# Kernel optimization log

Measured on AMD Instinct MI355X. Metric: run time of the kernel, lower is better.

The kernel has to match this reference:

```python
import jax, jax.numpy as jnp
import numpy as np

B, T, C = 4, 2048, 1024
H, D = 16, 64

def setup_inputs() -> dict:
    key = jax.random.key(0)
    k1, k2, k3 = jax.random.split(key, 3)
    x = jax.random.normal(k1, (B, T, C), dtype=jnp.float32)
    Wqkv = jax.random.normal(k2, (C, 3 * C), dtype=jnp.float32) * (1.0 / np.sqrt(C))
    Wproj = jax.random.normal(k3, (C, C), dtype=jnp.float32) * (1.0 / np.sqrt(C))
    return {"x": x, "Wqkv": Wqkv, "Wproj": Wproj}

def reference(x, Wqkv, Wproj):
    Bx, Tx, Cx = x.shape
    qkv = x @ Wqkv                       # (B, T, 3C)
    q, k, v = jnp.split(qkv, 3, axis=-1)
    # (B, T, C) -> (B, H, T, D)
    q = q.reshape(Bx, Tx, H, D).transpose(0, 2, 1, 3)
    k = k.reshape(Bx, Tx, H, D).transpose(0, 2, 1, 3)
    v = v.reshape(Bx, Tx, H, D).transpose(0, 2, 1, 3)
    att = jnp.einsum('bhqd,bhkd->bhqk', q, k) / jnp.sqrt(jnp.float32(D))
    causal = jnp.tril(jnp.ones((Tx, Tx), dtype=bool))  # (T, T)
    att = jnp.where(causal[None, None, :, :], att, jnp.float32(-jnp.inf))
    att = jax.nn.softmax(att, axis=-1)
    y = jnp.einsum('bhqk,bhkd->bhqd', att, v)          # (B, H, T, D)
    y = y.transpose(0, 2, 1, 3).reshape(Bx, Tx, Cx)
    return y @ Wproj
```

## Files before the change

kernel.cpp:

```cpp
#include <hip/hip_runtime.h>
#include <cstdint>
#include <cstddef>


typedef short bf16x8 __attribute__((ext_vector_type(8)));
typedef float f32x4 __attribute__((ext_vector_type(4)));
typedef float f32x16 __attribute__((ext_vector_type(16)));

#define MFMA32(a, b, c) __builtin_amdgcn_mfma_f32_16x16x32_bf16((a), (b), (c), 0, 0, 0)
#define MFMA3216(a, b, c) __builtin_amdgcn_mfma_f32_32x32x16_bf16((a), (b), (c), 0, 0, 0)

__device__ __forceinline__ unsigned short f2b(float f) {
  unsigned int x = __builtin_bit_cast(unsigned int, f);
  x += 0x7fffu + ((x >> 16) & 1u);
  return (unsigned short)(x >> 16);
}

__device__ __forceinline__ unsigned int pack2(float a, float b) {
  return (unsigned int)f2b(a) | ((unsigned int)f2b(b) << 16);
}

__device__ __forceinline__ unsigned int cvtpk(float a, float b) {
  unsigned int r;
  asm("v_cvt_pk_bf16_f32 %0, %1, %2" : "=v"(r) : "v"(a), "v"(b));
  return r;
}

__device__ __forceinline__ float exp2v(float x) {
  float r;
  asm("v_exp_f32 %0, %1" : "=v"(r) : "v"(x));
  return r;
}

__device__ __forceinline__ void gload16(const void* g, void* l) {
  __builtin_amdgcn_global_load_lds(
      (const __attribute__((address_space(1))) void*)g,
      (__attribute__((address_space(3))) void*)l, 16, 0, 0);
}

__global__ __launch_bounds__(256) void k_conv_x(const float* __restrict__ in,
                                                unsigned short* __restrict__ out, int n4) {
  int i = blockIdx.x * 256 + threadIdx.x;
  if (i >= n4) return;
  float4 v = reinterpret_cast<const float4*>(in)[i];
  ushort4 o;
  o.x = f2b(v.x); o.y = f2b(v.y); o.z = f2b(v.z); o.w = f2b(v.w);
  reinterpret_cast<ushort4*>(out)[i] = o;
}

__global__ __launch_bounds__(256) void k_transpose(const float* __restrict__ in,
                                                   unsigned short* __restrict__ out,
                                                   int R, int C) {
  __shared__ float tile[32][33];
  int c0 = blockIdx.x * 32, r0 = blockIdx.y * 32;
  int tx = threadIdx.x & 31, ty = threadIdx.x >> 5;
#pragma unroll
  for (int j = 0; j < 4; ++j)
    tile[ty + 8 * j][tx] = in[(size_t)(r0 + ty + 8 * j) * C + c0 + tx];
  __syncthreads();
#pragma unroll
  for (int j = 0; j < 4; ++j)
    out[(size_t)(c0 + ty + 8 * j) * R + r0 + tx] = f2b(tile[tx][ty + 8 * j]);
}

template <int EPI>
__global__ __launch_bounds__(256, 5) void k_gemm(const unsigned short* __restrict__ A,
                                                 const unsigned short* __restrict__ Bt,
                                                 float* __restrict__ outF,
                                                 unsigned short* __restrict__ q_ws,
                                                 unsigned short* __restrict__ k_ws,
                                                 unsigned short* __restrict__ v_ws,
                                                 int M, int N) {
  constexpr int K = 1024;
  __shared__ unsigned short smem[16384];
  unsigned short* As = smem;
  unsigned short* Bs = smem + 8192;
  const int bn = blockIdx.x, bm = blockIdx.y;
  const int tid = threadIdx.x;
  const int w = tid >> 6, lane = tid & 63;
  const int wm = w >> 1, wn = w & 1;
  const int c = lane & 15, g = lane >> 4;
  const int cl8 = c & 7;

  f32x4 acc[4][4];
#pragma unroll
  for (int i = 0; i < 4; ++i)
#pragma unroll
    for (int j = 0; j < 4; ++j) acc[i][j] = (f32x4){0.f, 0.f, 0.f, 0.f};

  const int srow = 32 * w + (lane >> 3);
  const int scol = 8 * ((lane & 7) ^ (lane >> 3));
  const unsigned short* Ag = A + (size_t)(bm * 128 + srow) * K + scol;
  const unsigned short* Bg = Bt + (size_t)(bn * 128 + srow) * K + scol;
  char* AsB = (char*)As + w * 4096;
  char* BsB = (char*)Bs + w * 4096;

  for (int kt = 0; kt < K / 64; ++kt) {
    const int kb = kt * 64;
    __syncthreads();
#pragma unroll
    for (int i = 0; i < 4; ++i) {
      gload16(Ag + (size_t)(8 * i) * K + kb, AsB + i * 1024);
      gload16(Bg + (size_t)(8 * i) * K + kb, BsB + i * 1024);
    }
    asm volatile("s_waitcnt vmcnt(0)" ::: "memory");
    __syncthreads();
#pragma unroll
    for (int u = 0; u < 2; ++u) {
      bf16x8 af[4], bfr[4];
#pragma unroll
      for (int mf = 0; mf < 4; ++mf)
        af[mf] = *(const bf16x8*)((const char*)As + (wm * 64 + mf * 16 + c) * 128 +
                                  (((u * 4 + g) ^ cl8) * 16));
#pragma unroll
      for (int nf = 0; nf < 4; ++nf)
        bfr[nf] = *(const bf16x8*)((const char*)Bs + (wn * 64 + nf * 16 + c) * 128 +
                                   (((u * 4 + g) ^ cl8) * 16));
#pragma unroll
      for (int mf = 0; mf < 4; ++mf)
#pragma unroll
        for (int nf = 0; nf < 4; ++nf)
          acc[mf][nf] = MFMA32(af[mf], bfr[nf], acc[mf][nf]);
    }
  }

  const int rowb = bm * 128 + wm * 64;
  const int colb = bn * 128 + wn * 64;
  if (EPI == 1) {
#pragma unroll
    for (int mf = 0; mf < 4; ++mf)
#pragma unroll
      for (int nf = 0; nf < 4; ++nf)
#pragma unroll
        for (int r = 0; r < 4; ++r) {
          int row = rowb + mf * 16 + 4 * g + r;
          int col = colb + nf * 16 + c;
          outF[(size_t)row * N + col] = acc[mf][nf][r];
        }
  } else {
    const int sec = colb >> 10;
    const int hh = (colb & 1023) >> 6;
    const int b = rowb >> 11, t0 = rowb & 2047;
    unsigned short* Lw = smem + w * 4096;

    __syncthreads();
    if (sec < 2) {
      const float sc = (sec == 0) ? 0.125f * 1.4426950408889634f : 1.f;
#pragma unroll
      for (int mf = 0; mf < 4; ++mf)
#pragma unroll
        for (int nf = 0; nf < 4; ++nf)
#pragma unroll
          for (int r = 0; r < 4; ++r)
            Lw[(16 * mf + 4 * g + r) * 64 + 16 * nf + c] = f2b(acc[mf][nf][r] * sc);
    } else {
#pragma unroll
      for (int mf = 0; mf < 4; ++mf)
#pragma unroll
        for (int nf = 0; nf < 4; ++nf)
#pragma unroll
          for (int rr = 0; rr < 2; ++rr)
            *(unsigned int*)&Lw[(16 * nf + c) * 64 + 16 * mf + 4 * g + 2 * rr] =
                pack2(acc[mf][nf][2 * rr], acc[mf][nf][2 * rr + 1]);
    }
    asm volatile("s_waitcnt lgkmcnt(0)" ::: "memory");
    const int rw = lane >> 3, ch = lane & 7;
    const int chx = ch ^ rw;
    if (sec == 0) {
      unsigned short* dst = q_ws + ((size_t)(b * 16 + hh) * 2048 + t0) * 64;
#pragma unroll
      for (int i = 0; i < 8; ++i) {
        int tl = i * 8 + rw;
        *(bf16x8*)(dst + (size_t)tl * 64 + ch * 8) = *(const bf16x8*)&Lw[tl * 64 + ch * 8];
      }
    } else if (sec == 1) {
      unsigned short* dst = k_ws + ((size_t)(b * 16 + hh) * 2048 + t0) * 64;
#pragma unroll
      for (int i = 0; i < 8; ++i) {
        int tl = i * 8 + rw;
        *(bf16x8*)(dst + (size_t)tl * 64 + chx * 8) = *(const bf16x8*)&Lw[tl * 64 + ch * 8];
      }
    } else {
      unsigned short* dst = v_ws + (size_t)(b * 16 + hh) * 64 * 2048 + t0;
#pragma unroll
      for (int i = 0; i < 8; ++i) {
        int dl = i * 8 + rw;
        *(bf16x8*)(dst + (size_t)dl * 2048 + chx * 8) = *(const bf16x8*)&Lw[dl * 64 + ch * 8];
      }
    }
  }
}

__global__ __launch_bounds__(256, 4) void k_attn(const unsigned short* __restrict__ q_ws,
                                                 const unsigned short* __restrict__ k_ws,
                                                 const unsigned short* __restrict__ v_ws,
                                                 unsigned short* __restrict__ y_ws) {
  constexpr int T = 2048;
  __shared__ unsigned short Ks[2][64 * 64];
  __shared__ unsigned short Vs[2][64 * 64];
  const int f = blockIdx.x;
  const int r = f >> 3;
  const int bh = (f & 7) * 8 + (r & 7);
  const int xi = 15 - (r >> 3);
  const int tid = threadIdx.x, w = tid >> 6, lane = tid & 63;
  const int q32 = lane & 31;
  const int hi = lane >> 5;
  const int l7 = lane & 7;
  const size_t base = (size_t)bh * T * 64;
  const unsigned short* Kb = k_ws + base;
  const unsigned short* Vb = v_ws + base;
  const unsigned short* Qb = q_ws + base;

  const int srow = w * 16 + (lane >> 3);
  const int sch = lane & 7;

  const int q0 = xi * 128;
  const int qb = q0 + 32 * w;
  const int qcol = qb + q32;
  const int n_kt = (q0 >> 6) + 2;
  bf16x8 qf[4];
#pragma unroll
  for (int ks = 0; ks < 4; ++ks)
    qf[ks] = *(const bf16x8*)(Qb + (size_t)qcol * 64 + 16 * ks + 8 * hi);

  f32x16 yacc[2];
#pragma unroll
  for (int db = 0; db < 2; ++db)
#pragma unroll
    for (int i = 0; i < 16; ++i) yacc[db][i] = 0.f;
  float m_run = -1e30f, l_part = 0.f;

  gload16(Kb + (size_t)srow * 64 + sch * 8, (char*)&Ks[0][0] + w * 2048);
  gload16(Kb + (size_t)(srow + 8) * 64 + sch * 8, (char*)&Ks[0][0] + w * 2048 + 1024);
  gload16(Vb + (size_t)srow * T + sch * 8, (char*)&Vs[0][0] + w * 2048);
  gload16(Vb + (size_t)(srow + 8) * T + sch * 8, (char*)&Vs[0][0] + w * 2048 + 1024);

#pragma unroll 1
  for (int kt = 0; kt < n_kt; ++kt) {
    const int k0 = kt * 64;
    const int cur = kt & 1;
    if (kt + 1 < n_kt) {
      const int k0n = k0 + 64;
      char* KsW = (char*)&Ks[cur ^ 1][0] + w * 2048;
      char* VsW = (char*)&Vs[cur ^ 1][0] + w * 2048;
      gload16(Kb + (size_t)(k0n + srow) * 64 + sch * 8, KsW);
      gload16(Kb + (size_t)(k0n + srow + 8) * 64 + sch * 8, KsW + 1024);
      gload16(Vb + (size_t)srow * T + k0n + sch * 8, VsW);
      gload16(Vb + (size_t)(srow + 8) * T + k0n + sch * 8, VsW + 1024);
      asm volatile("s_waitcnt vmcnt(4)" ::: "memory");
    } else {
      asm volatile("s_waitcnt vmcnt(0)" ::: "memory");
    }
    __builtin_amdgcn_s_barrier();

    if (k0 <= qb + 31) {
      const char* KsC = (const char*)&Ks[cur][0];
      const char* VsC = (const char*)&Vs[cur][0];
      f32x16 s[2];
#pragma unroll
      for (int tb = 0; tb < 2; ++tb)
#pragma unroll
        for (int i = 0; i < 16; ++i) s[tb][i] = 0.f;
      __builtin_amdgcn_s_setprio(1);
#pragma unroll
      for (int ks = 0; ks < 4; ++ks) {
        const int chk = ((2 * ks + hi) ^ l7) * 16;
#pragma unroll
        for (int tb = 0; tb < 2; ++tb) {
          const int row = 32 * tb + q32;
          bf16x8 kf = *(const bf16x8*)(KsC + row * 128 + chk);
          s[tb] = MFMA3216(kf, qf[ks], s[tb]);
        }
      }
      __builtin_amdgcn_s_setprio(0);
      if (k0 + 63 > qb) {
#pragma unroll
        for (int tb = 0; tb < 2; ++tb)
#pragma unroll
          for (int rr = 0; rr < 16; ++rr) {
            int tk = k0 + 32 * tb + (rr & 3) + 8 * (rr >> 2) + 4 * hi;
            if (tk > qcol) s[tb][rr] = -1e30f;
          }
      }
      float mx = s[0][0];
#pragma unroll
      for (int tb = 0; tb < 2; ++tb)
#pragma unroll
        for (int rr = 0; rr < 16; ++rr) mx = fmaxf(mx, s[tb][rr]);
      mx = fmaxf(mx, __shfl_xor(mx, 32));
      if (__any(mx > m_run + 11.5f)) {
        float m_new = fmaxf(m_run, mx);
        float corr = exp2v(m_run - m_new);
        l_part *= corr;
#pragma unroll
        for (int db = 0; db < 2; ++db)
#pragma unroll
          for (int i = 0; i < 16; ++i) yacc[db][i] *= corr;
        m_run = m_new;
      }
      unsigned pk[2][8];
      float ps = 0.f;
#pragma unroll
      for (int tb = 0; tb < 2; ++tb)
#pragma unroll
        for (int q4 = 0; q4 < 4; ++q4) {
          float p0 = exp2v(s[tb][4 * q4 + 0] - m_run);
          float p1 = exp2v(s[tb][4 * q4 + 1] - m_run);
          float p2 = exp2v(s[tb][4 * q4 + 2] - m_run);
          float p3 = exp2v(s[tb][4 * q4 + 3] - m_run);
          ps += ((p0 + p1) + (p2 + p3));
          pk[tb][2 * q4] = cvtpk(p0, p1);
          pk[tb][2 * q4 + 1] = cvtpk(p2, p3);
        }
      l_part += ps;

#pragma unroll
      for (int kw = 0; kw < 4; ++kw) {
        const int tb = kw >> 1, a = kw & 1;
        unsigned g00 = pk[tb][4 * a + 0], g01 = pk[tb][4 * a + 1];
        unsigned g10 = pk[tb][4 * a + 2], g11 = pk[tb][4 * a + 3];
        unsigned own0 = hi ? g10 : g00, own1 = hi ? g11 : g01;
        unsigned snd0 = hi ? g00 : g10, snd1 = hi ? g01 : g11;
        unsigned X0 = __shfl_xor(snd0, 32), X1 = __shfl_xor(snd1, 32);
        union { unsigned int u[4]; bf16x8 v; } pb;
        pb.u[0] = hi ? X0 : own0;
        pb.u[1] = hi ? X1 : own1;
        pb.u[2] = hi ? own0 : X0;
        pb.u[3] = hi ? own1 : X1;
        const int chv = ((2 * kw + hi) ^ l7) * 16;
        __builtin_amdgcn_s_setprio(1);
#pragma unroll
        for (int db = 0; db < 2; ++db) {
          const int row = 32 * db + q32;
          bf16x8 vf = *(const bf16x8*)(VsC + row * 128 + chv);
          yacc[db] = MFMA3216(vf, pb.v, yacc[db]);
        }
        __builtin_amdgcn_s_setprio(0);
      }
    }
    __builtin_amdgcn_s_barrier();
  }

  float lt = l_part + __shfl_xor(l_part, 32);
  float inv = 1.f / lt;
  const int b = bh >> 4, hh = bh & 15;
  unsigned short* yrow = y_ws + (size_t)(b * 2048 + qcol) * 1024 + hh * 64;
#pragma unroll
  for (int db = 0; db < 2; ++db)
#pragma unroll
    for (int rg = 0; rg < 4; ++rg) {
      uint2 o;
      o.x = cvtpk(yacc[db][4 * rg + 0] * inv, yacc[db][4 * rg + 1] * inv);
      o.y = cvtpk(yacc[db][4 * rg + 2] * inv, yacc[db][4 * rg + 3] * inv);
      *(uint2*)(yrow + 32 * db + 8 * rg + 4 * hi) = o;
    }
}

extern "C" void kernel_launch(void* const* d_in, const int* in_sizes, int n_in,
                              void* d_out, int out_size, void* d_ws, size_t ws_size,
                              hipStream_t stream) {
  const float* x = (const float*)d_in[0];
  const float* Wqkv = (const float*)d_in[1];
  const float* Wproj = (const float*)d_in[2];
  float* out = (float*)d_out;
  char* ws = (char*)d_ws;

  unsigned short* x_bf = (unsigned short*)(ws);
  unsigned short* wqkvT = (unsigned short*)(ws + 16777216);
  unsigned short* wprojT = (unsigned short*)(ws + 23068672);
  unsigned short* q_ws = (unsigned short*)(ws + 25165824);
  unsigned short* k_ws = (unsigned short*)(ws + 41943040);
  unsigned short* v_ws = (unsigned short*)(ws + 58720256);
  unsigned short* y_ws = (unsigned short*)(ws + 75497472);

  k_conv_x<<<8192, 256, 0, stream>>>(x, x_bf, 2097152);
  k_transpose<<<dim3(96, 32), 256, 0, stream>>>(Wqkv, wqkvT, 1024, 3072);
  k_transpose<<<dim3(32, 32), 256, 0, stream>>>(Wproj, wprojT, 1024, 1024);
  k_gemm<0><<<dim3(24, 64), 256, 0, stream>>>(x_bf, wqkvT, nullptr, q_ws, k_ws, v_ws, 8192, 3072);
  k_attn<<<1024, 256, 0, stream>>>(q_ws, k_ws, v_ws, y_ws);
  k_gemm<1><<<dim3(8, 64), 256, 0, stream>>>(y_ws, wprojT, out, nullptr, nullptr, nullptr, 8192, 1024);
}
```

Measured before the change: 172.9 us.

## Split long causal attention query tiles across two blocks and combine partials

Query tiles with index 8-15 (the longest causal KV ranges) are split into two blocks, each covering half of the key range, with a lookup-table schedule that interleaves long and short work. Each half writes unnormalized bf16 partial outputs plus running max and sum, and a new combine kernel merges them with log-sum-exp rescaling. This targets load imbalance and the tail of the attention grid. In exchange it adds an extra launch, partial-buffer traffic that reuses the x_bf and wqkvT workspace, and bf16 rounding of the unnormalized partials.

```diff
diff --git a/kernel.cpp b/kernel.cpp
--- a/kernel.cpp
+++ b/kernel.cpp
@@ -30,6 +30,11 @@
   float r;
   asm("v_exp_f32 %0, %1" : "=v"(r) : "v"(x));
   return r;
+}
+
+__device__ __forceinline__ float b2f(unsigned short u) {
+  unsigned int x = (unsigned int)u << 16;
+  return __builtin_bit_cast(float, x);
 }
 
 __device__ __forceinline__ void gload16(const void* g, void* l) {
@@ -194,14 +199,21 @@
 __global__ __launch_bounds__(256, 4) void k_attn(const unsigned short* __restrict__ q_ws,
                                                  const unsigned short* __restrict__ k_ws,
                                                  const unsigned short* __restrict__ v_ws,
-                                                 unsigned short* __restrict__ y_ws) {
+                                                 unsigned short* __restrict__ y_ws,
+                                                 unsigned short* __restrict__ part_y,
+                                                 float2* __restrict__ part_ml) {
   constexpr int T = 2048;
   __shared__ unsigned short Ks[2][64 * 64];
   __shared__ unsigned short Vs[2][64 * 64];
+  static constexpr signed char TXI[24] = {15, 15, 7, 14, 14, 13, 13, 6, 12, 12, 11, 11,
+                                          5, 10, 10, 9, 9, 4, 8, 8, 3, 2, 1, 0};
+  static constexpr signed char THF[24] = {0, 1, -1, 0, 1, 0, 1, -1, 0, 1, 0, 1,
+                                          -1, 0, 1, 0, 1, -1, 0, 1, -1, -1, -1, -1};
   const int f = blockIdx.x;
-  const int r = f >> 3;
-  const int bh = (f & 7) * 8 + (r & 7);
-  const int xi = 15 - (r >> 3);
+  const int cls = f >> 6;
+  const int bh = (f & 7) * 8 + ((f >> 3) & 7);
+  const int xi = TXI[cls];
+  const int half = THF[cls];
   const int tid = threadIdx.x, w = tid >> 6, lane = tid & 63;
   const int q32 = lane & 31;
   const int hi = lane >> 5;
@@ -217,7 +229,9 @@
   const int q0 = xi * 128;
   const int qb = q0 + 32 * w;
   const int qcol = qb + q32;
-  const int n_kt = (q0 >> 6) + 2;
+  const int nt = 2 * xi + 2;
+  const int kt_lo = (half == 1) ? (xi + 1) : 0;
+  const int kt_hi = (half == 0) ? (xi + 1) : nt;
   bf16x8 qf[4];
 #pragma unroll
   for (int ks = 0; ks < 4; ++ks)
@@ -230,16 +244,21 @@
     for (int i = 0; i < 16; ++i) yacc[db][i] = 0.f;
   float m_run = -1e30f, l_part = 0.f;
 
-  gload16(Kb + (size_t)srow * 64 + sch * 8, (char*)&Ks[0][0] + w * 2048);
-  gload16(Kb + (size_t)(srow + 8) * 64 + sch * 8, (char*)&Ks[0][0] + w * 2048 + 1024);
-  gload16(Vb + (size_t)srow * T + sch * 8, (char*)&Vs[0][0] + w * 2048);
-  gload16(Vb + (size_t)(srow + 8) * T + sch * 8, (char*)&Vs[0][0] + w * 2048 + 1024);
+  {
+    const int k0 = kt_lo * 64;
+    char* KsW = (char*)&Ks[kt_lo & 1][0] + w * 2048;
+    char* VsW = (char*)&Vs[kt_lo & 1][0] + w * 2048;
+    gload16(Kb + (size_t)(k0 + srow) * 64 + sch * 8, KsW);
+    gload16(Kb + (size_t)(k0 + srow + 8) * 64 + sch * 8, KsW + 1024);
+    gload16(Vb + (size_t)srow * T + k0 + sch * 8, VsW);
+    gload16(Vb + (size_t)(srow + 8) * T + k0 + sch * 8, VsW + 1024);
+  }
 
 #pragma unroll 1
-  for (int kt = 0; kt < n_kt; ++kt) {
+  for (int kt = kt_lo; kt < kt_hi; ++kt) {
     const int k0 = kt * 64;
     const int cur = kt & 1;
-    if (kt + 1 < n_kt) {
+    if (kt + 1 < kt_hi) {
       const int k0n = k0 + 64;
       char* KsW = (char*)&Ks[cur ^ 1][0] + w * 2048;
       char* VsW = (char*)&Vs[cur ^ 1][0] + w * 2048;
@@ -342,18 +361,65 @@
   }
 
   float lt = l_part + __shfl_xor(l_part, 32);
-  float inv = 1.f / lt;
+  const int rloc = 32 * w + q32;
+  if (half < 0) {
+    float inv = 1.f / lt;
+    const int b = bh >> 4, hh = bh & 15;
+    unsigned short* yrow = y_ws + (size_t)(b * 2048 + qcol) * 1024 + hh * 64;
+#pragma unroll
+    for (int db = 0; db < 2; ++db)
+#pragma unroll
+      for (int rg = 0; rg < 4; ++rg) {
+        uint2 o;
+        o.x = cvtpk(yacc[db][4 * rg + 0] * inv, yacc[db][4 * rg + 1] * inv);
+        o.y = cvtpk(yacc[db][4 * rg + 2] * inv, yacc[db][4 * rg + 3] * inv);
+        *(uint2*)(yrow + 32 * db + 8 * rg + 4 * hi) = o;
+      }
+  } else {
+    const int pt = ((bh << 3) + (xi - 8)) * 2 + half;
+    unsigned short* prow = part_y + (size_t)pt * 8192 + rloc * 64;
+#pragma unroll
+    for (int db = 0; db < 2; ++db)
+#pragma unroll
+      for (int rg = 0; rg < 4; ++rg) {
+        uint2 o;
+        o.x = cvtpk(yacc[db][4 * rg + 0], yacc[db][4 * rg + 1]);
+        o.y = cvtpk(yacc[db][4 * rg + 2], yacc[db][4 * rg + 3]);
+        *(uint2*)(prow + 32 * db + 8 * rg + 4 * hi) = o;
+      }
+    if (hi == 0) part_ml[pt * 128 + rloc] = make_float2(m_run, lt);
+  }
+}
+
+__global__ __launch_bounds__(256) void k_combine(const unsigned short* __restrict__ part_y,
+                                                 const float2* __restrict__ part_ml,
+                                                 unsigned short* __restrict__ y_ws) {
+  const int tile = blockIdx.x;
+  const int bh = tile >> 3;
+  const int xi = 8 + (tile & 7);
+  const int row = threadIdx.x >> 1;
+  const int dh = (threadIdx.x & 1) * 32;
+  const float2 A = part_ml[(tile * 2 + 0) * 128 + row];
+  const float2 B = part_ml[(tile * 2 + 1) * 128 + row];
+  const float m = fmaxf(A.x, B.x);
+  float eA = exp2v(A.x - m), eB = exp2v(B.x - m);
+  const float inv = 1.f / (A.y * eA + B.y * eB);
+  eA *= inv; eB *= inv;
+  const unsigned short* pa = part_y + (size_t)(tile * 2 + 0) * 8192 + row * 64 + dh;
+  const unsigned short* pb = part_y + (size_t)(tile * 2 + 1) * 8192 + row * 64 + dh;
   const int b = bh >> 4, hh = bh & 15;
-  unsigned short* yrow = y_ws + (size_t)(b * 2048 + qcol) * 1024 + hh * 64;
-#pragma unroll
-  for (int db = 0; db < 2; ++db)
-#pragma unroll
-    for (int rg = 0; rg < 4; ++rg) {
-      uint2 o;
-      o.x = cvtpk(yacc[db][4 * rg + 0] * inv, yacc[db][4 * rg + 1] * inv);
-      o.y = cvtpk(yacc[db][4 * rg + 2] * inv, yacc[db][4 * rg + 3] * inv);
-      *(uint2*)(yrow + 32 * db + 8 * rg + 4 * hi) = o;
-    }
+  unsigned short* o = y_ws + (size_t)(b * 2048 + xi * 128 + row) * 1024 + hh * 64 + dh;
+#pragma unroll
+  for (int i = 0; i < 4; ++i) {
+    bf16x8 a = *(const bf16x8*)(pa + 8 * i);
+    bf16x8 bb = *(const bf16x8*)(pb + 8 * i);
+    union { unsigned int u[4]; bf16x8 v; } r;
+#pragma unroll
+    for (int j = 0; j < 4; ++j)
+      r.u[j] = cvtpk(b2f((unsigned short)a[2 * j]) * eA + b2f((unsigned short)bb[2 * j]) * eB,
+                     b2f((unsigned short)a[2 * j + 1]) * eA + b2f((unsigned short)bb[2 * j + 1]) * eB);
+    *(bf16x8*)(o + 8 * i) = r.v;
+  }
 }
 
 extern "C" void kernel_launch(void* const* d_in, const int* in_sizes, int n_in,
@@ -373,10 +439,14 @@
   unsigned short* v_ws = (unsigned short*)(ws + 58720256);
   unsigned short* y_ws = (unsigned short*)(ws + 75497472);
 
+  unsigned short* part_y = x_bf;
+  float2* part_ml = (float2*)wqkvT;
+
   k_conv_x<<<8192, 256, 0, stream>>>(x, x_bf, 2097152);
   k_transpose<<<dim3(96, 32), 256, 0, stream>>>(Wqkv, wqkvT, 1024, 3072);
   k_transpose<<<dim3(32, 32), 256, 0, stream>>>(Wproj, wprojT, 1024, 1024);
   k_gemm<0><<<dim3(24, 64), 256, 0, stream>>>(x_bf, wqkvT, nullptr, q_ws, k_ws, v_ws, 8192, 3072);
-  k_attn<<<1024, 256, 0, stream>>>(q_ws, k_ws, v_ws, y_ws);
+  k_attn<<<1536, 256, 0, stream>>>(q_ws, k_ws, v_ws, y_ws, part_y, part_ml);
+  k_combine<<<512, 256, 0, stream>>>(part_y, part_ml, y_ws);
   k_gemm<1><<<dim3(8, 64), 256, 0, stream>>>(y_ws, wprojT, out, nullptr, nullptr, nullptr, 8192, 1024);
 }
```

Measured after the change: 179.3 us. +3.7%, slower.
